# Kernel tuning notes

Hardware: AMD Instinct MI355X
Metric: run time of the kernel (lower is better)

## Reference

```python
import jax, jax.numpy as jnp
import numpy as np

N_NODES = 10000
N_EDGES = 640000
F_IN = 128
F_HID = 128
BN_EPS = 1e-5


def _spectral_norm_weight(W, u):
    # One power iteration, matching torch.nn.utils.spectral_norm defaults.
    v = W.T @ u
    v = v / (jnp.linalg.norm(v) + 1e-12)
    u_new = W @ v
    u_new = u_new / (jnp.linalg.norm(u_new) + 1e-12)
    sigma = u_new @ (W @ v)
    return W / sigma


def setup_inputs() -> dict:
    key = jax.random.key(0)
    ks = jax.random.split(key, 8)
    x = jax.random.normal(ks[0], (N_NODES, F_IN), dtype=jnp.float32)
    edge_index = jax.random.randint(ks[1], (2, N_EDGES), 0, N_NODES, dtype=jnp.int64)
    W1 = jax.random.normal(ks[2], (F_HID, F_IN), dtype=jnp.float32) * (1.0 / np.sqrt(F_IN))
    b1 = jax.random.normal(ks[3], (F_HID,), dtype=jnp.float32) * 0.01
    u1 = jax.random.normal(ks[4], (F_HID,), dtype=jnp.float32)
    gamma = jnp.ones((F_HID,), dtype=jnp.float32)
    beta = jnp.zeros((F_HID,), dtype=jnp.float32)
    W2 = jax.random.normal(ks[5], (F_HID, F_HID), dtype=jnp.float32) * (1.0 / np.sqrt(F_HID))
    b2 = jax.random.normal(ks[6], (F_HID,), dtype=jnp.float32) * 0.01
    u2 = jax.random.normal(ks[7], (F_HID,), dtype=jnp.float32)
    return {"x": x, "edge_index": edge_index, "W1": W1, "b1": b1, "u1": u1,
            "gamma": gamma, "beta": beta, "W2": W2, "b2": b2, "u2": u2}


def reference(x, edge_index, W1, b1, u1, gamma, beta, W2, b2, u2):
    src, dst = edge_index[0], edge_index[1]
    # GINConv sum aggregation: out_i = sum_{j in N(i)} x_j
    agg = jax.ops.segment_sum(x[src], dst, num_segments=N_NODES)
    h = x + agg  # eps = 0 (default, train_eps=False)
    # MLP: SN-Linear -> ReLU -> BatchNorm1d (training stats) -> SN-Linear
    h = h @ _spectral_norm_weight(W1, u1).T + b1
    h = jax.nn.relu(h)
    mu = jnp.mean(h, axis=0)
    var = jnp.mean((h - mu) ** 2, axis=0)  # biased var, as torch BN forward
    h = gamma * (h - mu) / jnp.sqrt(var + BN_EPS) + beta
    h = h @ _spectral_norm_weight(W2, u2).T + b2
    return h
```

## Files before the change

### kernel.cpp

```cpp
#include <hip/hip_runtime.h>

#define NF 128
#define FB 64
#define MAXNODE 10240

__global__ __launch_bounds__(512) void power_iter_kernel(
    const float* __restrict__ W1, const float* __restrict__ u1,
    const float* __restrict__ W2, const float* __restrict__ u2,
    float* __restrict__ inv_sigma, float* __restrict__ W1t,
    float* __restrict__ colzero) {
    __shared__ float Wl[128][129];
    __shared__ float us[128], vv[128], part[4][128], red[128];
    int tid = threadIdx.x;

    const float* W = blockIdx.x ? W2 : W1;
    const float* u = blockIdx.x ? u2 : u1;
    const float4* W4 = (const float4*)W;
    for (int j = tid; j < 4096; j += 512) {
        float4 w = W4[j];
        int r = j >> 5, c0 = (j & 31) << 2;
        Wl[r][c0] = w.x; Wl[r][c0 + 1] = w.y; Wl[r][c0 + 2] = w.z; Wl[r][c0 + 3] = w.w;
    }
    if (tid < 128) us[tid] = u[tid];
    if (blockIdx.x == 0 && tid >= 256 && tid < 512) colzero[tid - 256] = 0.f;
    __syncthreads();

    int c = tid & 127, sl = tid >> 7;
    float acc = 0.f;
#pragma unroll
    for (int j = 0; j < 32; ++j) acc = fmaf(Wl[sl * 32 + j][c], us[sl * 32 + j], acc);
    part[sl][c] = acc;
    __syncthreads();
    if (tid < 128) {
        float v = part[0][tid] + part[1][tid] + part[2][tid] + part[3][tid];
        vv[tid] = v;
        red[tid] = v * v;
    }
    __syncthreads();
    for (int s = 64; s > 0; s >>= 1) { if (tid < s) red[tid] += red[tid + s]; __syncthreads(); }
    float nv = sqrtf(red[0]) + 1e-12f;
    __syncthreads();
    if (tid < 128) vv[tid] = vv[tid] / nv;
    __syncthreads();

    float t = 0.f;
#pragma unroll
    for (int k = 0; k < 32; ++k) t = fmaf(Wl[c][sl * 32 + k], vv[sl * 32 + k], t);
    part[sl][c] = t;
    __syncthreads();
    if (tid < 128) {
        float tv = part[0][tid] + part[1][tid] + part[2][tid] + part[3][tid];
        red[tid] = tv * tv;
    }
    __syncthreads();
    for (int s = 64; s > 0; s >>= 1) { if (tid < s) red[tid] += red[tid + s]; __syncthreads(); }
    float tt = red[0];
    float is = (sqrtf(tt) + 1e-12f) / tt;
    if (tid == 0) inv_sigma[blockIdx.x] = is;
    if (blockIdx.x == 0) {
        for (int idx = tid; idx < 16384; idx += 512) {
            int k = idx >> 7, j = idx & 127;
            W1t[idx] = Wl[j][k] * is;
        }
    }
}

__global__ __launch_bounds__(512) void hist_kernel(const int* __restrict__ dst, int n_edges,
                                                   int* __restrict__ hist2d, int nbin) {
    __shared__ int hist[MAXNODE];
    int tid = threadIdx.x, fb = blockIdx.x;
    for (int i = tid; i < nbin; i += 512) hist[i] = 0;
    __syncthreads();
    int chunk = (n_edges + FB - 1) / FB;
    int e0 = fb * chunk, e1 = min(e0 + chunk, n_edges);
    for (int e = e0 + tid; e < e1; e += 512) atomicAdd(&hist[dst[e]], 1);
    __syncthreads();
    for (int i = tid; i < nbin; i += 512) hist2d[(size_t)fb * nbin + i] = hist[i];
}

__global__ void scanA_kernel(int* __restrict__ hist2d, int* __restrict__ binOff, int nbin) {
    int bin = blockIdx.x * 1024 + threadIdx.x;
    if (bin >= nbin) return;
    int run = 0;
#pragma unroll 4
    for (int fb = 0; fb < FB; ++fb) {
        int v = hist2d[(size_t)fb * nbin + bin];
        hist2d[(size_t)fb * nbin + bin] = run;
        run += v;
    }
    binOff[bin] = run;
}

__global__ void scanB_kernel(int* __restrict__ binOff, int nbin) {
    __shared__ int sc[1024];
    int tid = threadIdx.x;
    int C = (nbin + 1023) >> 10;
    int b0 = tid * C, b1 = min(b0 + C, nbin);
    int loc[16];
    int s = 0;
    for (int i = b0; i < b1; ++i) { loc[i - b0] = binOff[i]; s += loc[i - b0]; }
    sc[tid] = s;
    __syncthreads();
    for (int off = 1; off < 1024; off <<= 1) {
        int v = (tid >= off) ? sc[tid - off] : 0;
        __syncthreads();
        sc[tid] += v;
        __syncthreads();
    }
    int base = sc[tid] - s;
    for (int i = b0; i < b1; ++i) { binOff[i] = base; base += loc[i - b0]; }
    if (tid == 1023) binOff[nbin] = sc[1023];
}

__global__ __launch_bounds__(512) void fill_kernel(
    const int* __restrict__ src, const int* __restrict__ dst,
    const int* __restrict__ hist2d, const int* __restrict__ binOff,
    int* __restrict__ bucket, int nbin, int n_edges) {
    __shared__ int cur[MAXNODE];
    int tid = threadIdx.x, fb = blockIdx.x;
    for (int i = tid; i < nbin; i += 512)
        cur[i] = hist2d[(size_t)fb * nbin + i] + binOff[i];
    __syncthreads();
    int chunk = (n_edges + FB - 1) / FB;
    int e0 = fb * chunk, e1 = min(e0 + chunk, n_edges);
    for (int e = e0 + tid; e < e1; e += 512) {
        int d = dst[e];
        int s = src[e];
        int pos = atomicAdd(&cur[d], 1);
        bucket[pos] = s;
    }
}

__global__ __launch_bounds__(256) void gather_kernel(
    const float* __restrict__ x, const int* __restrict__ bucket,
    const int* __restrict__ binOff, float* __restrict__ h0, int n_nodes) {
    int gw = (blockIdx.x * blockDim.x + threadIdx.x) >> 6;
    int lane = threadIdx.x & 63;
    if (gw >= n_nodes) return;
    const float2* x2 = (const float2*)x;
    float2 acc = x2[(size_t)gw * 64 + lane];
    int j = binOff[gw], end = binOff[gw + 1];
    for (; j + 4 <= end; j += 4) {
        int s0 = bucket[j], s1 = bucket[j + 1], s2 = bucket[j + 2], s3 = bucket[j + 3];
        float2 v0 = x2[(size_t)s0 * 64 + lane];
        float2 v1 = x2[(size_t)s1 * 64 + lane];
        float2 v2 = x2[(size_t)s2 * 64 + lane];
        float2 v3 = x2[(size_t)s3 * 64 + lane];
        acc.x += v0.x + v1.x + v2.x + v3.x;
        acc.y += v0.y + v1.y + v2.y + v3.y;
    }
    for (; j < end; ++j) {
        int s = bucket[j];
        float2 v = x2[(size_t)s * 64 + lane];
        acc.x += v.x;
        acc.y += v.y;
    }
    ((float2*)h0)[(size_t)gw * 64 + lane] = acc;
}

__global__ void edge_scatter_kernel(const int* __restrict__ ei, const float* __restrict__ x,
                                    float* __restrict__ h0, int n_edges) {
    int gtid = blockIdx.x * blockDim.x + threadIdx.x;
    int wid = gtid >> 6;
    int lane = threadIdx.x & 63;
    int nw = (gridDim.x * blockDim.x) >> 6;
    const int* srcs = ei;
    const int* dsts = ei + n_edges;
    for (int e = wid; e < n_edges; e += nw) {
        int s = srcs[e];
        int d = dsts[e];
        atomicAdd(&h0[d * NF + lane], x[s * NF + lane]);
        atomicAdd(&h0[d * NF + 64 + lane], x[s * NF + 64 + lane]);
    }
}

template <bool RELU, bool BNACC>
__global__ __launch_bounds__(256, 1) void gemm_tiled_kernel(
    const float* __restrict__ H, const float* __restrict__ Wt,
    const float* __restrict__ bias, float* __restrict__ O,
    float* __restrict__ colsum, float* __restrict__ colsumsq, int n_rows) {
    __shared__ float Hl[64][128];
    __shared__ float Wl[128][132];
    int tid = threadIdx.x;
    int m0 = blockIdx.x * 64;

    const float4* Wt4 = (const float4*)Wt;
    for (int j = tid; j < 4096; j += 256) {
        int k = j >> 5, c4 = (j & 31) << 2;
        float4 w = Wt4[j];
        *(float4*)&Wl[k][c4] = w;
    }
    const float4* H4 = (const float4*)H;
    for (int j = tid; j < 2048; j += 256) {
        int r = j >> 5, k4 = j & 31;
        int gr = m0 + r;
        float4 h = (gr < n_rows) ? H4[(size_t)gr * 32 + k4] : make_float4(0.f, 0.f, 0.f, 0.f);
        *(float4*)&Hl[r][k4 << 2] = h;
    }
    __syncthreads();

    int tx = tid & 31, ty = tid >> 5;
    int rb = ty * 8, cb = tx * 4;
    float acc[8][4] = {};

    for (int k = 0; k < 128; k += 4) {
        float wv[4][4];
#pragma unroll
        for (int kk = 0; kk < 4; ++kk) {
            float4 t = *(const float4*)&Wl[k + kk][cb];
            wv[kk][0] = t.x; wv[kk][1] = t.y; wv[kk][2] = t.z; wv[kk][3] = t.w;
        }
#pragma unroll
        for (int i = 0; i < 8; ++i) {
            float4 h = *(const float4*)&Hl[rb + i][k];
            float hf[4] = {h.x, h.y, h.z, h.w};
#pragma unroll
            for (int kk = 0; kk < 4; ++kk)
#pragma unroll
                for (int j = 0; j < 4; ++j)
                    acc[i][j] = fmaf(hf[kk], wv[kk][j], acc[i][j]);
        }
    }

    float bv[4];
#pragma unroll
    for (int j = 0; j < 4; ++j) bv[j] = bias[cb + j];

    float s[4] = {0.f, 0.f, 0.f, 0.f}, q[4] = {0.f, 0.f, 0.f, 0.f};
#pragma unroll
    for (int i = 0; i < 8; ++i) {
        int gr = m0 + rb + i;
        if (gr < n_rows) {
            float o[4];
#pragma unroll
            for (int j = 0; j < 4; ++j) {
                float v = acc[i][j] + bv[j];
                if (RELU) v = fmaxf(v, 0.f);
                o[j] = v;
                if (BNACC) { s[j] += v; q[j] = fmaf(v, v, q[j]); }
            }
            *(float4*)&O[(size_t)gr * NF + cb] = make_float4(o[0], o[1], o[2], o[3]);
        }
    }

    if (BNACC) {
        __syncthreads();
        float* sS = &Hl[0][0];
        float* sQ = &Hl[16][0];
#pragma unroll
        for (int j = 0; j < 4; ++j) {
            sS[ty * 128 + cb + j] = s[j];
            sQ[ty * 128 + cb + j] = q[j];
        }
        __syncthreads();
        if (tid < 128) {
            float ts = 0.f, tq = 0.f;
#pragma unroll
            for (int g = 0; g < 8; ++g) {
                ts += sS[g * 128 + tid];
                tq += sQ[g * 128 + tid];
            }
            atomicAdd(&colsum[tid], ts);
            atomicAdd(&colsumsq[tid], tq);
        }
    }
}

__global__ void fold_kernel(const float* __restrict__ W2, const float* __restrict__ b2,
                            const float* __restrict__ gamma, const float* __restrict__ beta,
                            const float* __restrict__ colsum, const float* __restrict__ colsumsq,
                            const float* __restrict__ inv_sigma, float* __restrict__ W2pt,
                            float* __restrict__ b2p, float inv_n) {
    __shared__ float a[128], cc[128], red[128];
    int k = threadIdx.x;
    int j = blockIdx.x;
    float mu = colsum[k] * inv_n;
    float var = colsumsq[k] * inv_n - mu * mu;
    float ai = gamma[k] / sqrtf(var + 1e-5f);
    a[k] = ai;
    cc[k] = beta[k] - ai * mu;
    __syncthreads();
    float is2 = inv_sigma[1];
    float wv = W2[j * 128 + k] * is2;
    W2pt[k * 128 + j] = wv * a[k];
    red[k] = wv * cc[k];
    __syncthreads();
    for (int s = 64; s > 0; s >>= 1) { if (k < s) red[k] += red[k + s]; __syncthreads(); }
    if (k == 0) b2p[j] = b2[j] + red[0];
}

extern "C" void kernel_launch(void* const* d_in, const int* in_sizes, int n_in,
                              void* d_out, int out_size, void* d_ws, size_t ws_size,
                              hipStream_t stream) {
    const float* x     = (const float*)d_in[0];
    const int*   ei    = (const int*)d_in[1];
    const float* W1    = (const float*)d_in[2];
    const float* b1    = (const float*)d_in[3];
    const float* u1    = (const float*)d_in[4];
    const float* gamma = (const float*)d_in[5];
    const float* beta  = (const float*)d_in[6];
    const float* W2    = (const float*)d_in[7];
    const float* b2    = (const float*)d_in[8];
    const float* u2    = (const float*)d_in[9];
    float* out = (float*)d_out;

    int n_nodes = in_sizes[0] / NF;
    int n_edges = in_sizes[1] / 2;
    int nbin = n_nodes;

    float* ws        = (float*)d_ws;
    float* inv_sigma = ws;
    float* colsum    = ws + 4;
    float* colsumsq  = colsum + 128;
    float* W1t       = colsumsq + 128;
    float* W2pt      = W1t + 16384;
    float* b2p       = W2pt + 16384;
    int*   binOff    = (int*)(b2p + 128);
    int*   bucket    = binOff + nbin + 1;
    float* h0        = (float*)(bucket + n_edges);
    int*   hist2d    = (int*)h0;

    size_t fixed = (4 + 256 + 2 * 16384 + 128) * sizeof(float);
    size_t need  = fixed + ((size_t)nbin + 1 + n_edges) * sizeof(int)
                 + (size_t)n_nodes * NF * sizeof(float);
    bool fused = (n_nodes <= MAXNODE) && (ws_size >= need)
               && ((size_t)FB * nbin <= (size_t)n_nodes * NF);

    power_iter_kernel<<<2, 512, 0, stream>>>(W1, u1, W2, u2, inv_sigma, W1t, colsum);

    if (fused) {
        hist_kernel<<<FB, 512, 0, stream>>>(ei + n_edges, n_edges, hist2d, nbin);
        scanA_kernel<<<(nbin + 1023) / 1024, 1024, 0, stream>>>(hist2d, binOff, nbin);
        scanB_kernel<<<1, 1024, 0, stream>>>(binOff, nbin);
        fill_kernel<<<FB, 512, 0, stream>>>(ei, ei + n_edges, hist2d, binOff, bucket,
                                            nbin, n_edges);
        gather_kernel<<<(n_nodes * 64 + 255) / 256, 256, 0, stream>>>(
            x, bucket, binOff, h0, n_nodes);
    } else {
        hipMemcpyAsync(h0, x, (size_t)n_nodes * NF * sizeof(float),
                       hipMemcpyDeviceToDevice, stream);
        edge_scatter_kernel<<<2048, 256, 0, stream>>>(ei, x, h0, n_edges);
    }

    int gemm_blocks = (n_nodes + 63) / 64;

    gemm_tiled_kernel<true, true><<<gemm_blocks, 256, 0, stream>>>(
        h0, W1t, b1, out, colsum, colsumsq, n_nodes);

    fold_kernel<<<128, 128, 0, stream>>>(W2, b2, gamma, beta, colsum, colsumsq,
                                         inv_sigma, W2pt, b2p, 1.0f / (float)n_nodes);

    gemm_tiled_kernel<false, false><<<gemm_blocks, 256, 0, stream>>>(
        out, W2pt, b2p, out, nullptr, nullptr, n_nodes);
}
```

Measured before the change: 131.4 us.

## Fuse power iteration with histogram, fold BN into GEMM2, vectorize CSR build

Merges the spectral-norm power iteration and the destination histogram into one launch. It also doubles the number of histogram and fill blocks, and replaces the single-block scan with a wave-shuffle scan. The histogram and fill loops read int4, and the gather loop is unrolled to 8 neighbours. The BN fold now runs inside the second GEMM, so each block recomputes the folded W2 and bias, which drops a separate kernel and a workspace round trip. The price is redundant per-block fold work, shared-memory float atomics for the bias, and a larger hist2d (FB=128) that still has to fit in h0.

```diff
diff --git a/kernel.cpp b/kernel.cpp
--- a/kernel.cpp
+++ b/kernel.cpp
@@ -1,17 +1,44 @@
 #include <hip/hip_runtime.h>
 
 #define NF 128
-#define FB 64
+#define FB 128
 #define MAXNODE 10240
 
-__global__ __launch_bounds__(512) void power_iter_kernel(
+__global__ __launch_bounds__(512) void power_hist_kernel(
     const float* __restrict__ W1, const float* __restrict__ u1,
     const float* __restrict__ W2, const float* __restrict__ u2,
+    const int* __restrict__ dst, int n_edges,
+    int* __restrict__ hist2d, int nbin,
     float* __restrict__ inv_sigma, float* __restrict__ W1t,
     float* __restrict__ colzero) {
     __shared__ float Wl[128][129];
     __shared__ float us[128], vv[128], part[4][128], red[128];
+    __shared__ int hist[MAXNODE];
     int tid = threadIdx.x;
+
+    if (blockIdx.x >= 2) {
+        int fb = blockIdx.x - 2;
+        for (int i = tid; i < nbin; i += 512) hist[i] = 0;
+        __syncthreads();
+        int chunk = (n_edges + FB - 1) / FB;
+        int e0 = fb * chunk, e1 = min(e0 + chunk, n_edges);
+        int a0 = min(e1, (e0 + 3) & ~3);
+        for (int e = e0 + tid; e < a0; e += 512) atomicAdd(&hist[dst[e]], 1);
+        const int4* d4 = (const int4*)dst;
+        int vs = a0 >> 2, ve = e1 >> 2;
+        for (int i = vs + tid; i < ve; i += 512) {
+            int4 d = d4[i];
+            atomicAdd(&hist[d.x], 1);
+            atomicAdd(&hist[d.y], 1);
+            atomicAdd(&hist[d.z], 1);
+            atomicAdd(&hist[d.w], 1);
+        }
+        for (int e = (ve << 2) + tid; e < e1; e += 512)
+            if (e >= a0) atomicAdd(&hist[dst[e]], 1);
+        __syncthreads();
+        for (int i = tid; i < nbin; i += 512) hist2d[(size_t)fb * nbin + i] = hist[i];
+        return;
+    }
 
     const float* W = blockIdx.x ? W2 : W1;
     const float* u = blockIdx.x ? u2 : u1;
@@ -63,19 +90,6 @@
             W1t[idx] = Wl[j][k] * is;
         }
     }
-}
-
-__global__ __launch_bounds__(512) void hist_kernel(const int* __restrict__ dst, int n_edges,
-                                                   int* __restrict__ hist2d, int nbin) {
-    __shared__ int hist[MAXNODE];
-    int tid = threadIdx.x, fb = blockIdx.x;
-    for (int i = tid; i < nbin; i += 512) hist[i] = 0;
-    __syncthreads();
-    int chunk = (n_edges + FB - 1) / FB;
-    int e0 = fb * chunk, e1 = min(e0 + chunk, n_edges);
-    for (int e = e0 + tid; e < e1; e += 512) atomicAdd(&hist[dst[e]], 1);
-    __syncthreads();
-    for (int i = tid; i < nbin; i += 512) hist2d[(size_t)fb * nbin + i] = hist[i];
 }
 
 __global__ void scanA_kernel(int* __restrict__ hist2d, int* __restrict__ binOff, int nbin) {
@@ -91,25 +105,40 @@
     binOff[bin] = run;
 }
 
-__global__ void scanB_kernel(int* __restrict__ binOff, int nbin) {
-    __shared__ int sc[1024];
-    int tid = threadIdx.x;
-    int C = (nbin + 1023) >> 10;
-    int b0 = tid * C, b1 = min(b0 + C, nbin);
-    int loc[16];
-    int s = 0;
-    for (int i = b0; i < b1; ++i) { loc[i - b0] = binOff[i]; s += loc[i - b0]; }
-    sc[tid] = s;
-    __syncthreads();
-    for (int off = 1; off < 1024; off <<= 1) {
-        int v = (tid >= off) ? sc[tid - off] : 0;
-        __syncthreads();
-        sc[tid] += v;
-        __syncthreads();
-    }
-    int base = sc[tid] - s;
-    for (int i = b0; i < b1; ++i) { binOff[i] = base; base += loc[i - b0]; }
-    if (tid == 1023) binOff[nbin] = sc[1023];
+__global__ __launch_bounds__(1024) void scanB_kernel(int* __restrict__ binOff, int nbin) {
+    __shared__ int wsum[16], wexcl[16];
+    __shared__ int carry_s;
+    int tid = threadIdx.x, lane = tid & 63, wv = tid >> 6;
+    if (tid == 0) carry_s = 0;
+    __syncthreads();
+    int nr = (nbin + 1023) >> 10;
+    for (int r = 0; r < nr; ++r) {
+        int i = (r << 10) + tid;
+        int v = (i < nbin) ? binOff[i] : 0;
+        int inc = v;
+        for (int off = 1; off < 64; off <<= 1) {
+            int t = __shfl_up(inc, off);
+            if (lane >= off) inc += t;
+        }
+        if (lane == 63) wsum[wv] = inc;
+        __syncthreads();
+        if (wv == 0) {
+            int s = (lane < 16) ? wsum[lane] : 0;
+            int si = s;
+            for (int off = 1; off < 16; off <<= 1) {
+                int t = __shfl_up(si, off);
+                if (lane >= off) si += t;
+            }
+            if (lane < 16) wexcl[lane] = si - s;
+        }
+        __syncthreads();
+        int excl = inc - v + wexcl[wv] + carry_s;
+        if (i < nbin) binOff[i] = excl;
+        __syncthreads();
+        if (tid == 1023) carry_s += wexcl[15] + wsum[15];
+        __syncthreads();
+    }
+    if (threadIdx.x == 0) binOff[nbin] = carry_s;
 }
 
 __global__ __launch_bounds__(512) void fill_kernel(
@@ -123,12 +152,28 @@
     __syncthreads();
     int chunk = (n_edges + FB - 1) / FB;
     int e0 = fb * chunk, e1 = min(e0 + chunk, n_edges);
-    for (int e = e0 + tid; e < e1; e += 512) {
-        int d = dst[e];
-        int s = src[e];
-        int pos = atomicAdd(&cur[d], 1);
-        bucket[pos] = s;
-    }
+    int a0 = min(e1, (e0 + 3) & ~3);
+    for (int e = e0 + tid; e < a0; e += 512) {
+        int pos = atomicAdd(&cur[dst[e]], 1);
+        bucket[pos] = src[e];
+    }
+    const int4* d4 = (const int4*)dst;
+    const int4* s4 = (const int4*)src;
+    int vs = a0 >> 2, ve = e1 >> 2;
+    for (int i = vs + tid; i < ve; i += 512) {
+        int4 d = d4[i];
+        int4 s = s4[i];
+        int p0 = atomicAdd(&cur[d.x], 1);
+        int p1 = atomicAdd(&cur[d.y], 1);
+        int p2 = atomicAdd(&cur[d.z], 1);
+        int p3 = atomicAdd(&cur[d.w], 1);
+        bucket[p0] = s.x; bucket[p1] = s.y; bucket[p2] = s.z; bucket[p3] = s.w;
+    }
+    for (int e = (ve << 2) + tid; e < e1; e += 512)
+        if (e >= a0) {
+            int pos = atomicAdd(&cur[dst[e]], 1);
+            bucket[pos] = src[e];
+        }
 }
 
 __global__ __launch_bounds__(256) void gather_kernel(
@@ -140,14 +185,19 @@
     const float2* x2 = (const float2*)x;
     float2 acc = x2[(size_t)gw * 64 + lane];
     int j = binOff[gw], end = binOff[gw + 1];
-    for (; j + 4 <= end; j += 4) {
-        int s0 = bucket[j], s1 = bucket[j + 1], s2 = bucket[j + 2], s3 = bucket[j + 3];
+    for (; j + 8 <= end; j += 8) {
+        int s0 = bucket[j],     s1 = bucket[j + 1], s2 = bucket[j + 2], s3 = bucket[j + 3];
+        int s4 = bucket[j + 4], s5 = bucket[j + 5], s6 = bucket[j + 6], s7 = bucket[j + 7];
         float2 v0 = x2[(size_t)s0 * 64 + lane];
         float2 v1 = x2[(size_t)s1 * 64 + lane];
         float2 v2 = x2[(size_t)s2 * 64 + lane];
         float2 v3 = x2[(size_t)s3 * 64 + lane];
-        acc.x += v0.x + v1.x + v2.x + v3.x;
-        acc.y += v0.y + v1.y + v2.y + v3.y;
+        float2 v4 = x2[(size_t)s4 * 64 + lane];
+        float2 v5 = x2[(size_t)s5 * 64 + lane];
+        float2 v6 = x2[(size_t)s6 * 64 + lane];
+        float2 v7 = x2[(size_t)s7 * 64 + lane];
+        acc.x += ((v0.x + v1.x) + (v2.x + v3.x)) + ((v4.x + v5.x) + (v6.x + v7.x));
+        acc.y += ((v0.y + v1.y) + (v2.y + v3.y)) + ((v4.y + v5.y) + (v6.y + v7.y));
     }
     for (; j < end; ++j) {
         int s = bucket[j];
@@ -174,8 +224,7 @@
     }
 }
 
-template <bool RELU, bool BNACC>
-__global__ __launch_bounds__(256, 1) void gemm_tiled_kernel(
+__global__ __launch_bounds__(256, 1) void gemm1_kernel(
     const float* __restrict__ H, const float* __restrict__ Wt,
     const float* __restrict__ bias, float* __restrict__ O,
     float* __restrict__ colsum, float* __restrict__ colsumsq, int n_rows) {
@@ -235,58 +284,117 @@
 #pragma unroll
             for (int j = 0; j < 4; ++j) {
                 float v = acc[i][j] + bv[j];
-                if (RELU) v = fmaxf(v, 0.f);
+                v = fmaxf(v, 0.f);
                 o[j] = v;
-                if (BNACC) { s[j] += v; q[j] = fmaf(v, v, q[j]); }
+                s[j] += v;
+                q[j] = fmaf(v, v, q[j]);
             }
             *(float4*)&O[(size_t)gr * NF + cb] = make_float4(o[0], o[1], o[2], o[3]);
         }
     }
 
-    if (BNACC) {
-        __syncthreads();
-        float* sS = &Hl[0][0];
-        float* sQ = &Hl[16][0];
-#pragma unroll
-        for (int j = 0; j < 4; ++j) {
-            sS[ty * 128 + cb + j] = s[j];
-            sQ[ty * 128 + cb + j] = q[j];
-        }
-        __syncthreads();
-        if (tid < 128) {
-            float ts = 0.f, tq = 0.f;
-#pragma unroll
-            for (int g = 0; g < 8; ++g) {
-                ts += sS[g * 128 + tid];
-                tq += sQ[g * 128 + tid];
-            }
-            atomicAdd(&colsum[tid], ts);
-            atomicAdd(&colsumsq[tid], tq);
-        }
-    }
-}
-
-__global__ void fold_kernel(const float* __restrict__ W2, const float* __restrict__ b2,
-                            const float* __restrict__ gamma, const float* __restrict__ beta,
-                            const float* __restrict__ colsum, const float* __restrict__ colsumsq,
-                            const float* __restrict__ inv_sigma, float* __restrict__ W2pt,
-                            float* __restrict__ b2p, float inv_n) {
-    __shared__ float a[128], cc[128], red[128];
-    int k = threadIdx.x;
-    int j = blockIdx.x;
-    float mu = colsum[k] * inv_n;
-    float var = colsumsq[k] * inv_n - mu * mu;
-    float ai = gamma[k] / sqrtf(var + 1e-5f);
-    a[k] = ai;
-    cc[k] = beta[k] - ai * mu;
-    __syncthreads();
+    __syncthreads();
+    float* sS = &Hl[0][0];
+    float* sQ = &Hl[16][0];
+#pragma unroll
+    for (int j = 0; j < 4; ++j) {
+        sS[ty * 128 + cb + j] = s[j];
+        sQ[ty * 128 + cb + j] = q[j];
+    }
+    __syncthreads();
+    if (tid < 128) {
+        float ts = 0.f, tq = 0.f;
+#pragma unroll
+        for (int g = 0; g < 8; ++g) {
+            ts += sS[g * 128 + tid];
+            tq += sQ[g * 128 + tid];
+        }
+        atomicAdd(&colsum[tid], ts);
+        atomicAdd(&colsumsq[tid], tq);
+    }
+}
+
+__global__ __launch_bounds__(256, 1) void gemm2_fold_kernel(
+    const float* __restrict__ H, const float* __restrict__ W2,
+    const float* __restrict__ b2, const float* __restrict__ gamma,
+    const float* __restrict__ beta, const float* __restrict__ colsum,
+    const float* __restrict__ colsumsq, const float* __restrict__ inv_sigma,
+    float* __restrict__ O, int n_rows, float inv_n) {
+    __shared__ float Hl[64][128];
+    __shared__ float Wl[128][132];
+    __shared__ float a_s[128], c_s[128], bsh[128];
+    int tid = threadIdx.x;
+    int m0 = blockIdx.x * 64;
+
+    if (tid < 128) {
+        float mu = colsum[tid] * inv_n;
+        float var = colsumsq[tid] * inv_n - mu * mu;
+        float ai = gamma[tid] / sqrtf(var + 1e-5f);
+        a_s[tid] = ai;
+        c_s[tid] = beta[tid] - ai * mu;
+        bsh[tid] = 0.f;
+    }
+    const float4* H4 = (const float4*)H;
+    for (int j = tid; j < 2048; j += 256) {
+        int r = j >> 5, k4 = j & 31;
+        int gr = m0 + r;
+        float4 h = (gr < n_rows) ? H4[(size_t)gr * 32 + k4] : make_float4(0.f, 0.f, 0.f, 0.f);
+        *(float4*)&Hl[r][k4 << 2] = h;
+    }
+    __syncthreads();
+
     float is2 = inv_sigma[1];
-    float wv = W2[j * 128 + k] * is2;
-    W2pt[k * 128 + j] = wv * a[k];
-    red[k] = wv * cc[k];
-    __syncthreads();
-    for (int s = 64; s > 0; s >>= 1) { if (k < s) red[k] += red[k + s]; __syncthreads(); }
-    if (k == 0) b2p[j] = b2[j] + red[0];
+    const float4* W4 = (const float4*)W2;
+    for (int idx = tid; idx < 4096; idx += 256) {
+        int j = idx & 127, k4 = idx >> 7, k = k4 << 2;
+        float4 w = W4[j * 32 + k4];
+        w.x *= is2; w.y *= is2; w.z *= is2; w.w *= is2;
+        Wl[k][j]     = w.x * a_s[k];
+        Wl[k + 1][j] = w.y * a_s[k + 1];
+        Wl[k + 2][j] = w.z * a_s[k + 2];
+        Wl[k + 3][j] = w.w * a_s[k + 3];
+        float pb = w.x * c_s[k] + w.y * c_s[k + 1] + w.z * c_s[k + 2] + w.w * c_s[k + 3];
+        atomicAdd(&bsh[j], pb);
+    }
+    __syncthreads();
+
+    int tx = tid & 31, ty = tid >> 5;
+    int rb = ty * 8, cb = tx * 4;
+    float acc[8][4] = {};
+
+    for (int k = 0; k < 128; k += 4) {
+        float wv[4][4];
+#pragma unroll
+        for (int kk = 0; kk < 4; ++kk) {
+            float4 t = *(const float4*)&Wl[k + kk][cb];
+            wv[kk][0] = t.x; wv[kk][1] = t.y; wv[kk][2] = t.z; wv[kk][3] = t.w;
+        }
+#pragma unroll
+        for (int i = 0; i < 8; ++i) {
+            float4 h = *(const float4*)&Hl[rb + i][k];
+            float hf[4] = {h.x, h.y, h.z, h.w};
+#pragma unroll
+            for (int kk = 0; kk < 4; ++kk)
+#pragma unroll
+                for (int j = 0; j < 4; ++j)
+                    acc[i][j] = fmaf(hf[kk], wv[kk][j], acc[i][j]);
+        }
+    }
+
+    float bv[4];
+#pragma unroll
+    for (int j = 0; j < 4; ++j) bv[j] = b2[cb + j] + bsh[cb + j];
+
+#pragma unroll
+    for (int i = 0; i < 8; ++i) {
+        int gr = m0 + rb + i;
+        if (gr < n_rows) {
+            float o[4];
+#pragma unroll
+            for (int j = 0; j < 4; ++j) o[j] = acc[i][j] + bv[j];
+            *(float4*)&O[(size_t)gr * NF + cb] = make_float4(o[0], o[1], o[2], o[3]);
+        }
+    }
 }
 
 extern "C" void kernel_launch(void* const* d_in, const int* in_sizes, int n_in,
@@ -313,23 +421,20 @@
     float* colsum    = ws + 4;
     float* colsumsq  = colsum + 128;
     float* W1t       = colsumsq + 128;
-    float* W2pt      = W1t + 16384;
-    float* b2p       = W2pt + 16384;
-    int*   binOff    = (int*)(b2p + 128);
+    int*   binOff    = (int*)(W1t + 16384);
     int*   bucket    = binOff + nbin + 1;
     float* h0        = (float*)(bucket + n_edges);
     int*   hist2d    = (int*)h0;
 
-    size_t fixed = (4 + 256 + 2 * 16384 + 128) * sizeof(float);
+    size_t fixed = (4 + 256 + 16384) * sizeof(float);
     size_t need  = fixed + ((size_t)nbin + 1 + n_edges) * sizeof(int)
                  + (size_t)n_nodes * NF * sizeof(float);
     bool fused = (n_nodes <= MAXNODE) && (ws_size >= need)
                && ((size_t)FB * nbin <= (size_t)n_nodes * NF);
 
-    power_iter_kernel<<<2, 512, 0, stream>>>(W1, u1, W2, u2, inv_sigma, W1t, colsum);
-
     if (fused) {
-        hist_kernel<<<FB, 512, 0, stream>>>(ei + n_edges, n_edges, hist2d, nbin);
+        power_hist_kernel<<<2 + FB, 512, 0, stream>>>(
+            W1, u1, W2, u2, ei + n_edges, n_edges, hist2d, nbin, inv_sigma, W1t, colsum);
         scanA_kernel<<<(nbin + 1023) / 1024, 1024, 0, stream>>>(hist2d, binOff, nbin);
         scanB_kernel<<<1, 1024, 0, stream>>>(binOff, nbin);
         fill_kernel<<<FB, 512, 0, stream>>>(ei, ei + n_edges, hist2d, binOff, bucket,
@@ -337,6 +442,8 @@
         gather_kernel<<<(n_nodes * 64 + 255) / 256, 256, 0, stream>>>(
             x, bucket, binOff, h0, n_nodes);
     } else {
+        power_hist_kernel<<<2, 512, 0, stream>>>(
+            W1, u1, W2, u2, ei + n_edges, n_edges, nullptr, nbin, inv_sigma, W1t, colsum);
         hipMemcpyAsync(h0, x, (size_t)n_nodes * NF * sizeof(float),
                        hipMemcpyDeviceToDevice, stream);
         edge_scatter_kernel<<<2048, 256, 0, stream>>>(ei, x, h0, n_edges);
@@ -344,12 +451,9 @@
 
     int gemm_blocks = (n_nodes + 63) / 64;
 
-    gemm_tiled_kernel<true, true><<<gemm_blocks, 256, 0, stream>>>(
-        h0, W1t, b1, out, colsum, colsumsq, n_nodes);
-
-    fold_kernel<<<128, 128, 0, stream>>>(W2, b2, gamma, beta, colsum, colsumsq,
-                                         inv_sigma, W2pt, b2p, 1.0f / (float)n_nodes);
-
-    gemm_tiled_kernel<false, false><<<gemm_blocks, 256, 0, stream>>>(
-        out, W2pt, b2p, out, nullptr, nullptr, n_nodes);
-}
+    gemm1_kernel<<<gemm_blocks, 256, 0, stream>>>(h0, W1t, b1, out, colsum, colsumsq, n_nodes);
+
+    gemm2_fold_kernel<<<gemm_blocks, 256, 0, stream>>>(
+        out, W2, b2, gamma, beta, colsum, colsumsq, inv_sigma, out, n_nodes,
+        1.0f / (float)n_nodes);
+}
```

New measurement: 126.2 us. 1.04x faster.

## Gather from bf16 copy of x, fuse power-iteration with histogram, vectorize CSR build

Applied to the files above, without the earlier changes.

Converts x to bf16 inside a merged launch that also runs the power iteration and the dst histogram, then gathers neighbour rows from the bf16 copy to halve gather traffic. The histogram and fill loops now read indices as int4, FB doubles to 128, scanB becomes a wave-shuffle scan, and the GEMM reads W straight from global memory instead of LDS to raise occupancy. The bf16 neighbour features cost accuracy in the aggregation sum, and a larger FB means more partial histograms to scan.

```diff
diff --git a/kernel.cpp b/kernel.cpp
--- a/kernel.cpp
+++ b/kernel.cpp
@@ -1,17 +1,64 @@
 #include <hip/hip_runtime.h>
 
 #define NF 128
-#define FB 64
+#define FB 128
+#define CB 64
 #define MAXNODE 10240
 
-__global__ __launch_bounds__(512) void power_iter_kernel(
+__device__ __forceinline__ unsigned short f2bf(float f) {
+    unsigned int u = __float_as_uint(f);
+    unsigned int r = u + 0x7FFFu + ((u >> 16) & 1u);
+    return (unsigned short)(r >> 16);
+}
+
+__global__ __launch_bounds__(512) void power_hist_kernel(
     const float* __restrict__ W1, const float* __restrict__ u1,
     const float* __restrict__ W2, const float* __restrict__ u2,
+    const int* __restrict__ dst, int n_edges,
+    int* __restrict__ hist2d, int nbin,
+    const float* __restrict__ x, unsigned short* __restrict__ xb, int n_x4,
     float* __restrict__ inv_sigma, float* __restrict__ W1t,
     float* __restrict__ colzero) {
     __shared__ float Wl[128][129];
     __shared__ float us[128], vv[128], part[4][128], red[128];
+    __shared__ int hist[MAXNODE];
     int tid = threadIdx.x;
+
+    if (blockIdx.x >= 2 + FB) {
+        int cb = blockIdx.x - 2 - FB;
+        const float4* x4 = (const float4*)x;
+        ushort4* xb4 = (ushort4*)xb;
+        for (int i = cb * 512 + tid; i < n_x4; i += CB * 512) {
+            float4 v = x4[i];
+            ushort4 o;
+            o.x = f2bf(v.x); o.y = f2bf(v.y); o.z = f2bf(v.z); o.w = f2bf(v.w);
+            xb4[i] = o;
+        }
+        return;
+    }
+    if (blockIdx.x >= 2) {
+        int fb = blockIdx.x - 2;
+        for (int i = tid; i < nbin; i += 512) hist[i] = 0;
+        __syncthreads();
+        int chunk = (n_edges + FB - 1) / FB;
+        int e0 = fb * chunk, e1 = min(e0 + chunk, n_edges);
+        int a0 = min(e1, (e0 + 3) & ~3);
+        for (int e = e0 + tid; e < a0; e += 512) atomicAdd(&hist[dst[e]], 1);
+        const int4* d4 = (const int4*)dst;
+        int vs = a0 >> 2, ve = e1 >> 2;
+        for (int i = vs + tid; i < ve; i += 512) {
+            int4 d = d4[i];
+            atomicAdd(&hist[d.x], 1);
+            atomicAdd(&hist[d.y], 1);
+            atomicAdd(&hist[d.z], 1);
+            atomicAdd(&hist[d.w], 1);
+        }
+        for (int e = (ve << 2) + tid; e < e1; e += 512)
+            if (e >= a0) atomicAdd(&hist[dst[e]], 1);
+        __syncthreads();
+        for (int i = tid; i < nbin; i += 512) hist2d[(size_t)fb * nbin + i] = hist[i];
+        return;
+    }
 
     const float* W = blockIdx.x ? W2 : W1;
     const float* u = blockIdx.x ? u2 : u1;
@@ -63,19 +110,6 @@
             W1t[idx] = Wl[j][k] * is;
         }
     }
-}
-
-__global__ __launch_bounds__(512) void hist_kernel(const int* __restrict__ dst, int n_edges,
-                                                   int* __restrict__ hist2d, int nbin) {
-    __shared__ int hist[MAXNODE];
-    int tid = threadIdx.x, fb = blockIdx.x;
-    for (int i = tid; i < nbin; i += 512) hist[i] = 0;
-    __syncthreads();
-    int chunk = (n_edges + FB - 1) / FB;
-    int e0 = fb * chunk, e1 = min(e0 + chunk, n_edges);
-    for (int e = e0 + tid; e < e1; e += 512) atomicAdd(&hist[dst[e]], 1);
-    __syncthreads();
-    for (int i = tid; i < nbin; i += 512) hist2d[(size_t)fb * nbin + i] = hist[i];
 }
 
 __global__ void scanA_kernel(int* __restrict__ hist2d, int* __restrict__ binOff, int nbin) {
@@ -91,25 +125,40 @@
     binOff[bin] = run;
 }
 
-__global__ void scanB_kernel(int* __restrict__ binOff, int nbin) {
-    __shared__ int sc[1024];
-    int tid = threadIdx.x;
-    int C = (nbin + 1023) >> 10;
-    int b0 = tid * C, b1 = min(b0 + C, nbin);
-    int loc[16];
-    int s = 0;
-    for (int i = b0; i < b1; ++i) { loc[i - b0] = binOff[i]; s += loc[i - b0]; }
-    sc[tid] = s;
-    __syncthreads();
-    for (int off = 1; off < 1024; off <<= 1) {
-        int v = (tid >= off) ? sc[tid - off] : 0;
-        __syncthreads();
-        sc[tid] += v;
-        __syncthreads();
-    }
-    int base = sc[tid] - s;
-    for (int i = b0; i < b1; ++i) { binOff[i] = base; base += loc[i - b0]; }
-    if (tid == 1023) binOff[nbin] = sc[1023];
+__global__ __launch_bounds__(1024) void scanB_kernel(int* __restrict__ binOff, int nbin) {
+    __shared__ int wsum[16], wexcl[16];
+    __shared__ int carry_s;
+    int tid = threadIdx.x, lane = tid & 63, wv = tid >> 6;
+    if (tid == 0) carry_s = 0;
+    __syncthreads();
+    int nr = (nbin + 1023) >> 10;
+    for (int r = 0; r < nr; ++r) {
+        int i = (r << 10) + tid;
+        int v = (i < nbin) ? binOff[i] : 0;
+        int inc = v;
+        for (int off = 1; off < 64; off <<= 1) {
+            int t = __shfl_up(inc, off);
+            if (lane >= off) inc += t;
+        }
+        if (lane == 63) wsum[wv] = inc;
+        __syncthreads();
+        if (wv == 0) {
+            int s = (lane < 16) ? wsum[lane] : 0;
+            int si = s;
+            for (int off = 1; off < 16; off <<= 1) {
+                int t = __shfl_up(si, off);
+                if (lane >= off) si += t;
+            }
+            if (lane < 16) wexcl[lane] = si - s;
+        }
+        __syncthreads();
+        int excl = inc - v + wexcl[wv] + carry_s;
+        if (i < nbin) binOff[i] = excl;
+        __syncthreads();
+        if (tid == 1023) carry_s += wexcl[15] + wsum[15];
+        __syncthreads();
+    }
+    if (threadIdx.x == 0) binOff[nbin] = carry_s;
 }
 
 __global__ __launch_bounds__(512) void fill_kernel(
@@ -123,37 +172,66 @@
     __syncthreads();
     int chunk = (n_edges + FB - 1) / FB;
     int e0 = fb * chunk, e1 = min(e0 + chunk, n_edges);
-    for (int e = e0 + tid; e < e1; e += 512) {
-        int d = dst[e];
-        int s = src[e];
-        int pos = atomicAdd(&cur[d], 1);
-        bucket[pos] = s;
-    }
+    int a0 = min(e1, (e0 + 3) & ~3);
+    for (int e = e0 + tid; e < a0; e += 512) {
+        int pos = atomicAdd(&cur[dst[e]], 1);
+        bucket[pos] = src[e];
+    }
+    const int4* d4 = (const int4*)dst;
+    const int4* s4 = (const int4*)src;
+    int vs = a0 >> 2, ve = e1 >> 2;
+    for (int i = vs + tid; i < ve; i += 512) {
+        int4 d = d4[i];
+        int4 s = s4[i];
+        int p0 = atomicAdd(&cur[d.x], 1);
+        int p1 = atomicAdd(&cur[d.y], 1);
+        int p2 = atomicAdd(&cur[d.z], 1);
+        int p3 = atomicAdd(&cur[d.w], 1);
+        bucket[p0] = s.x; bucket[p1] = s.y; bucket[p2] = s.z; bucket[p3] = s.w;
+    }
+    for (int e = (ve << 2) + tid; e < e1; e += 512)
+        if (e >= a0) {
+            int pos = atomicAdd(&cur[dst[e]], 1);
+            bucket[pos] = src[e];
+        }
 }
 
 __global__ __launch_bounds__(256) void gather_kernel(
-    const float* __restrict__ x, const int* __restrict__ bucket,
+    const unsigned short* __restrict__ xb, const int* __restrict__ bucket,
     const int* __restrict__ binOff, float* __restrict__ h0, int n_nodes) {
     int gw = (blockIdx.x * blockDim.x + threadIdx.x) >> 6;
     int lane = threadIdx.x & 63;
     if (gw >= n_nodes) return;
-    const float2* x2 = (const float2*)x;
-    float2 acc = x2[(size_t)gw * 64 + lane];
+    const unsigned int* xu = (const unsigned int*)xb;
+    unsigned int u0 = xu[(size_t)gw * 64 + lane];
+    float2 acc;
+    acc.x = __uint_as_float(u0 << 16);
+    acc.y = __uint_as_float(u0 & 0xFFFF0000u);
     int j = binOff[gw], end = binOff[gw + 1];
-    for (; j + 4 <= end; j += 4) {
-        int s0 = bucket[j], s1 = bucket[j + 1], s2 = bucket[j + 2], s3 = bucket[j + 3];
-        float2 v0 = x2[(size_t)s0 * 64 + lane];
-        float2 v1 = x2[(size_t)s1 * 64 + lane];
-        float2 v2 = x2[(size_t)s2 * 64 + lane];
-        float2 v3 = x2[(size_t)s3 * 64 + lane];
-        acc.x += v0.x + v1.x + v2.x + v3.x;
-        acc.y += v0.y + v1.y + v2.y + v3.y;
+    for (; j + 8 <= end; j += 8) {
+        int s0 = bucket[j],     s1 = bucket[j + 1], s2 = bucket[j + 2], s3 = bucket[j + 3];
+        int s4 = bucket[j + 4], s5 = bucket[j + 5], s6 = bucket[j + 6], s7 = bucket[j + 7];
+        unsigned int v0 = xu[(size_t)s0 * 64 + lane];
+        unsigned int v1 = xu[(size_t)s1 * 64 + lane];
+        unsigned int v2 = xu[(size_t)s2 * 64 + lane];
+        unsigned int v3 = xu[(size_t)s3 * 64 + lane];
+        unsigned int v4 = xu[(size_t)s4 * 64 + lane];
+        unsigned int v5 = xu[(size_t)s5 * 64 + lane];
+        unsigned int v6 = xu[(size_t)s6 * 64 + lane];
+        unsigned int v7 = xu[(size_t)s7 * 64 + lane];
+        acc.x += __uint_as_float(v0 << 16) + __uint_as_float(v1 << 16)
+               + __uint_as_float(v2 << 16) + __uint_as_float(v3 << 16)
+               + __uint_as_float(v4 << 16) + __uint_as_float(v5 << 16)
+               + __uint_as_float(v6 << 16) + __uint_as_float(v7 << 16);
+        acc.y += __uint_as_float(v0 & 0xFFFF0000u) + __uint_as_float(v1 & 0xFFFF0000u)
+               + __uint_as_float(v2 & 0xFFFF0000u) + __uint_as_float(v3 & 0xFFFF0000u)
+               + __uint_as_float(v4 & 0xFFFF0000u) + __uint_as_float(v5 & 0xFFFF0000u)
+               + __uint_as_float(v6 & 0xFFFF0000u) + __uint_as_float(v7 & 0xFFFF0000u);
     }
     for (; j < end; ++j) {
-        int s = bucket[j];
-        float2 v = x2[(size_t)s * 64 + lane];
-        acc.x += v.x;
-        acc.y += v.y;
+        unsigned int v = xu[(size_t)bucket[j] * 64 + lane];
+        acc.x += __uint_as_float(v << 16);
+        acc.y += __uint_as_float(v & 0xFFFF0000u);
     }
     ((float2*)h0)[(size_t)gw * 64 + lane] = acc;
 }
@@ -175,21 +253,14 @@
 }
 
 template <bool RELU, bool BNACC>
-__global__ __launch_bounds__(256, 1) void gemm_tiled_kernel(
+__global__ __launch_bounds__(256, 4) void gemm_kernel(
     const float* __restrict__ H, const float* __restrict__ Wt,
     const float* __restrict__ bias, float* __restrict__ O,
     float* __restrict__ colsum, float* __restrict__ colsumsq, int n_rows) {
     __shared__ float Hl[64][128];
-    __shared__ float Wl[128][132];
     int tid = threadIdx.x;
     int m0 = blockIdx.x * 64;
 
-    const float4* Wt4 = (const float4*)Wt;
-    for (int j = tid; j < 4096; j += 256) {
-        int k = j >> 5, c4 = (j & 31) << 2;
-        float4 w = Wt4[j];
-        *(float4*)&Wl[k][c4] = w;
-    }
     const float4* H4 = (const float4*)H;
     for (int j = tid; j < 2048; j += 256) {
         int r = j >> 5, k4 = j & 31;
@@ -202,14 +273,16 @@
     int tx = tid & 31, ty = tid >> 5;
     int rb = ty * 8, cb = tx * 4;
     float acc[8][4] = {};
-
+    const float4* Wt4 = (const float4*)Wt;
+
+#pragma unroll 2
     for (int k = 0; k < 128; k += 4) {
-        float wv[4][4];
-#pragma unroll
-        for (int kk = 0; kk < 4; ++kk) {
-            float4 t = *(const float4*)&Wl[k + kk][cb];
-            wv[kk][0] = t.x; wv[kk][1] = t.y; wv[kk][2] = t.z; wv[kk][3] = t.w;
-        }
+        float4 w0 = Wt4[(k + 0) * 32 + tx];
+        float4 w1 = Wt4[(k + 1) * 32 + tx];
+        float4 w2 = Wt4[(k + 2) * 32 + tx];
+        float4 w3 = Wt4[(k + 3) * 32 + tx];
+        float wv[4][4] = {{w0.x, w0.y, w0.z, w0.w}, {w1.x, w1.y, w1.z, w1.w},
+                          {w2.x, w2.y, w2.z, w2.w}, {w3.x, w3.y, w3.z, w3.w}};
 #pragma unroll
         for (int i = 0; i < 8; ++i) {
             float4 h = *(const float4*)&Hl[rb + i][k];
@@ -307,6 +380,8 @@
     int n_nodes = in_sizes[0] / NF;
     int n_edges = in_sizes[1] / 2;
     int nbin = n_nodes;
+    int nbin_pad = (nbin + 1 + 3) & ~3;
+    int nedge_pad = (n_edges + 3) & ~3;
 
     float* ws        = (float*)d_ws;
     float* inv_sigma = ws;
@@ -316,27 +391,32 @@
     float* W2pt      = W1t + 16384;
     float* b2p       = W2pt + 16384;
     int*   binOff    = (int*)(b2p + 128);
-    int*   bucket    = binOff + nbin + 1;
-    float* h0        = (float*)(bucket + n_edges);
+    int*   bucket    = binOff + nbin_pad;
+    float* h0        = (float*)(bucket + nedge_pad);
+    unsigned short* xb = (unsigned short*)(h0 + (size_t)n_nodes * NF);
     int*   hist2d    = (int*)h0;
 
-    size_t fixed = (4 + 256 + 2 * 16384 + 128) * sizeof(float);
-    size_t need  = fixed + ((size_t)nbin + 1 + n_edges) * sizeof(int)
-                 + (size_t)n_nodes * NF * sizeof(float);
+    size_t need = (size_t)(33156 + nbin_pad + nedge_pad) * 4
+                + (size_t)n_nodes * NF * 4 + (size_t)n_nodes * NF * 2;
     bool fused = (n_nodes <= MAXNODE) && (ws_size >= need)
                && ((size_t)FB * nbin <= (size_t)n_nodes * NF);
 
-    power_iter_kernel<<<2, 512, 0, stream>>>(W1, u1, W2, u2, inv_sigma, W1t, colsum);
+    int n_x4 = n_nodes * 32;
 
     if (fused) {
-        hist_kernel<<<FB, 512, 0, stream>>>(ei + n_edges, n_edges, hist2d, nbin);
+        power_hist_kernel<<<2 + FB + CB, 512, 0, stream>>>(
+            W1, u1, W2, u2, ei + n_edges, n_edges, hist2d, nbin,
+            x, xb, n_x4, inv_sigma, W1t, colsum);
         scanA_kernel<<<(nbin + 1023) / 1024, 1024, 0, stream>>>(hist2d, binOff, nbin);
         scanB_kernel<<<1, 1024, 0, stream>>>(binOff, nbin);
         fill_kernel<<<FB, 512, 0, stream>>>(ei, ei + n_edges, hist2d, binOff, bucket,
                                             nbin, n_edges);
         gather_kernel<<<(n_nodes * 64 + 255) / 256, 256, 0, stream>>>(
-            x, bucket, binOff, h0, n_nodes);
+            xb, bucket, binOff, h0, n_nodes);
     } else {
+        power_hist_kernel<<<2, 512, 0, stream>>>(
+            W1, u1, W2, u2, ei + n_edges, n_edges, nullptr, nbin,
+            x, xb, 0, inv_sigma, W1t, colsum);
         hipMemcpyAsync(h0, x, (size_t)n_nodes * NF * sizeof(float),
                        hipMemcpyDeviceToDevice, stream);
         edge_scatter_kernel<<<2048, 256, 0, stream>>>(ei, x, h0, n_edges);
@@ -344,12 +424,12 @@
 
     int gemm_blocks = (n_nodes + 63) / 64;
 
-    gemm_tiled_kernel<true, true><<<gemm_blocks, 256, 0, stream>>>(
+    gemm_kernel<true, true><<<gemm_blocks, 256, 0, stream>>>(
         h0, W1t, b1, out, colsum, colsumsq, n_nodes);
 
     fold_kernel<<<128, 128, 0, stream>>>(W2, b2, gamma, beta, colsum, colsumsq,
                                          inv_sigma, W2pt, b2p, 1.0f / (float)n_nodes);
 
-    gemm_tiled_kernel<false, false><<<gemm_blocks, 256, 0, stream>>>(
+    gemm_kernel<false, false><<<gemm_blocks, 256, 0, stream>>>(
         out, W2pt, b2p, out, nullptr, nullptr, n_nodes);
 }
```

After: 112.8 us. 14.1% less time.
